# Optimization experiments

Measured on AMD Instinct MI355X. Metric: run time of the kernel, lower is better.

## Reference

```python
import jax, jax.numpy as jnp
import numpy as np

SIG_LEVEL = 2
UNIT = 128
SEQ = 64
BATCH = 256
SIG_DIM = UNIT + UNIT ** 2  # truncated signature dim for level 2
LN_EPS = 1e-5


def _signature(path, level):
    """Truncated path signature up to `level` via Chen's relation.
    path: (B, T, d) -> (B, d + d^2 + ... + d^level).
    Each segment contributes exp(dx): level-m term dx^{outer m}/m!.
    """
    B, T, d = path.shape
    dx = path[:, 1:] - path[:, :-1]  # (B, T-1, d)
    init = [jnp.zeros((B, d ** k), dtype=path.dtype) for k in range(1, level + 1)]

    def step(S, dxt):  # S: list of (B, d^k); dxt: (B, d)
        # P[m] = dxt^{outer m} / m!, flattened (B, d^m)
        P = [jnp.ones((B, 1), dtype=dxt.dtype), dxt]
        for m in range(2, level + 1):
            P.append((P[-1][:, :, None] * dxt[:, None, :]).reshape(B, d ** m) / m)
        newS = []
        for k in range(1, level + 1):
            s = P[k]  # j = 0 term (S_0 = 1)
            for j in range(1, k + 1):
                s = s + (S[j - 1][:, :, None] * P[k - j][:, None, :]).reshape(B, d ** k)
            newS.append(s)
        return newS, None

    S, _ = jax.lax.scan(step, init, jnp.swapaxes(dx, 0, 1))
    return jnp.concatenate(S, axis=-1)


def _grn_softmax(sig, W2, b2, W1, b1, Wg, bg, Wv, bv, Ws, bs, gamma, beta):
    # TFT-style gated residual network with softmax output activation.
    h = jax.nn.elu(sig @ W2 + b2)          # (B, unit)
    h = h @ W1 + b1                        # (B, unit)
    glu = jax.nn.sigmoid(h @ Wg + bg) * (h @ Wv + bv)
    skip = sig @ Ws + bs                   # residual projection sig_dim -> unit
    y = skip + glu
    mu = jnp.mean(y, axis=-1, keepdims=True)
    var = jnp.var(y, axis=-1, keepdims=True)
    y = (y - mu) * jax.lax.rsqrt(var + LN_EPS) * gamma + beta
    return jax.nn.softmax(y, axis=-1)


def setup_inputs() -> dict:
    key = jax.random.key(0)
    ks = jax.random.split(key, 16)
    s = 0.02
    return {
        "inputs": jax.random.normal(ks[0], (BATCH, SEQ, UNIT), dtype=jnp.float32),
        "time_kernel": jnp.ones((SEQ, 1), dtype=jnp.float32),
        "Wd": jax.random.normal(ks[1], (UNIT, UNIT), dtype=jnp.float32) * s,
        "bd": jnp.zeros((UNIT,), dtype=jnp.float32),
        "W2": jax.random.normal(ks[2], (SIG_DIM, UNIT), dtype=jnp.float32) * s,
        "b2": jnp.zeros((UNIT,), dtype=jnp.float32),
        "W1": jax.random.normal(ks[3], (UNIT, UNIT), dtype=jnp.float32) * s,
        "b1": jnp.zeros((UNIT,), dtype=jnp.float32),
        "Wg": jax.random.normal(ks[4], (UNIT, UNIT), dtype=jnp.float32) * s,
        "bg": jnp.zeros((UNIT,), dtype=jnp.float32),
        "Wv": jax.random.normal(ks[5], (UNIT, UNIT), dtype=jnp.float32) * s,
        "bv": jnp.zeros((UNIT,), dtype=jnp.float32),
        "Ws": jax.random.normal(ks[6], (SIG_DIM, UNIT), dtype=jnp.float32) * s,
        "bs": jnp.zeros((UNIT,), dtype=jnp.float32),
        "gamma": jnp.ones((UNIT,), dtype=jnp.float32),
        "beta": jnp.zeros((UNIT,), dtype=jnp.float32),
    }


def reference(inputs, time_kernel, Wd, bd, W2, b2, W1, b1, Wg, bg, Wv, bv, Ws, bs, gamma, beta):
    x = time_kernel * inputs                         # (B, T, d) time weighting
    sig = _signature(x, SIG_LEVEL)                   # (B, sig_dim)
    weights = _grn_softmax(sig, W2, b2, W1, b1, Wg, bg, Wv, bv, Ws, bs, gamma, beta)  # (B, d)
    dense_out = x @ Wd + bd                          # (B, T, d); dropout is identity at eval
    return dense_out * weights[:, None, :]
```

## Files before the change

kernel.cpp:

```cpp
#include <hip/hip_runtime.h>
#include <math.h>

#define SD 16512
#define NCH 32
#define NKB 516
#define RPSTRIDE 8192
#define LN_EPS 1e-5f

typedef __attribute__((ext_vector_type(4))) float f32x4;
typedef __attribute__((ext_vector_type(8))) short bf16x8;

__device__ __forceinline__ unsigned bfpack(float lo, float hi) {
    unsigned a = __builtin_bit_cast(unsigned, lo);
    unsigned b = __builtin_bit_cast(unsigned, hi);
    a = (a + 0x7FFFu + ((a >> 16) & 1u)) >> 16;
    b = (b + 0x7FFFu + ((b >> 16) & 1u)) >> 16;
    return a | (b << 16);
}
__device__ __forceinline__ unsigned short bf1(float x) {
    unsigned a = __builtin_bit_cast(unsigned, x);
    return (unsigned short)((a + 0x7FFFu + ((a >> 16) & 1u)) >> 16);
}

__global__ __launch_bounds__(512) void k_sig(const float* __restrict__ x,
                                             const float* __restrict__ tk,
                                             const float* __restrict__ Wd,
                                             const float* __restrict__ W2,
                                             const float* __restrict__ Ws,
                                             unsigned short* __restrict__ sigF,
                                             unsigned short* __restrict__ WTgF,
                                             unsigned short* __restrict__ xbf,
                                             unsigned short* __restrict__ WdTg) {
    __shared__ union {
        struct { unsigned short Ut[128][72]; unsigned short DXt[128][72]; float tks[64]; } s;
        struct { float T[32][132]; } t;
    } sm;
    int tid = threadIdx.x;
    int p = blockIdx.x;

    if (p >= 256 && p < 1288) {
        int q = p - 256;
        int mat = q & 1, kblk = q >> 1;
        int k0 = kblk * 32;
        const float* Wm = mat ? Ws : W2;
        {
            int kk = tid >> 4, c0 = (tid & 15) * 8;
            const float* src = Wm + (size_t)(k0 + kk) * 128 + c0;
            f32x4 v0 = *(const f32x4*)src;
            f32x4 v1 = *(const f32x4*)(src + 4);
            #pragma unroll
            for (int j = 0; j < 4; ++j) sm.t.T[kk][c0 + j]     = v0[j];
            #pragma unroll
            for (int j = 0; j < 4; ++j) sm.t.T[kk][c0 + 4 + j] = v1[j];
        }
        __syncthreads();
        {
            int c = tid >> 2, h8 = (tid & 3) * 8;
            uint4 o;
            o.x = bfpack(sm.t.T[h8    ][c], sm.t.T[h8 + 1][c]);
            o.y = bfpack(sm.t.T[h8 + 2][c], sm.t.T[h8 + 3][c]);
            o.z = bfpack(sm.t.T[h8 + 4][c], sm.t.T[h8 + 5][c]);
            o.w = bfpack(sm.t.T[h8 + 6][c], sm.t.T[h8 + 7][c]);
            *(uint4*)&WTgF[((size_t)(mat * NKB + kblk) * 128 + c) * 32 + h8] = o;
        }
        return;
    }
    if (p == 1288) {
        int d = tid & 127, kh = tid >> 7;
        unsigned* dst = (unsigned*)WdTg;
        for (int kk = 0; kk < 32; kk += 2) {
            int k = kh * 32 + kk;
            float v0 = Wd[(size_t)k * 128 + d];
            float v1 = Wd[(size_t)(k + 1) * 128 + d];
            dst[d * 64 + (k >> 1)] = bfpack(v0, v1);
        }
        return;
    }

    int b = p;
    if (tid < 64) sm.s.tks[tid] = tk[tid];
    __syncthreads();

    const float* xb = x + (size_t)b * 8192;
    unsigned short* xbb = xbf + (size_t)b * 8192;
    int i = tid & 127, th = tid >> 7;

    float x0 = sm.s.tks[0] * xb[i];
    float xa = sm.s.tks[th * 16] * xb[(size_t)(th * 16) * 128 + i];
    #pragma unroll
    for (int tp = 0; tp < 8; ++tp) {
        int pp = th * 8 + tp;
        int t0 = 2 * pp;
        float xv = sm.s.tks[t0 + 1] * xb[(size_t)(t0 + 1) * 128 + i];
        float dx0 = xv - xa, u0 = 0.5f * (xa + xv) - x0;
        float dx1, u1, xc;
        if (pp == 31) { dx1 = 0.f; u1 = 0.f; xc = 0.f; }
        else {
            xc = sm.s.tks[t0 + 2] * xb[(size_t)(t0 + 2) * 128 + i];
            dx1 = xc - xv; u1 = 0.5f * (xv + xc) - x0;
        }
        *(unsigned*)&sm.s.Ut[i][t0]  = bfpack(u0, u1);
        *(unsigned*)&sm.s.DXt[i][t0] = bfpack(dx0, dx1);
        xbb[(size_t)t0 * 128 + i]       = bf1(xa);
        xbb[(size_t)(t0 + 1) * 128 + i] = bf1(xv);
        if (pp == 31)
            sigF[(size_t)(i >> 5) * 8192 + b * 32 + (i & 31)] = bf1(xv - x0);
        xa = xc;
    }
    __syncthreads();

    int w = tid >> 6, lane = tid & 63;
    int wm = w >> 2, wn = w & 3;
    int l15 = lane & 15, lg = lane >> 4;
    f32x4 acc[4][2];
    #pragma unroll
    for (int m = 0; m < 4; ++m)
        #pragma unroll
        for (int n = 0; n < 2; ++n) acc[m][n] = (f32x4){0.f, 0.f, 0.f, 0.f};

    #pragma unroll
    for (int ks = 0; ks < 2; ++ks) {
        bf16x8 af[4], bfv[2];
        #pragma unroll
        for (int m = 0; m < 4; ++m)
            af[m] = *(const bf16x8*)&sm.s.Ut[wm * 64 + m * 16 + l15][ks * 32 + lg * 8];
        #pragma unroll
        for (int n = 0; n < 2; ++n)
            bfv[n] = *(const bf16x8*)&sm.s.DXt[wn * 32 + n * 16 + l15][ks * 32 + lg * 8];
        #pragma unroll
        for (int m = 0; m < 4; ++m)
            #pragma unroll
            for (int n = 0; n < 2; ++n)
                acc[m][n] = __builtin_amdgcn_mfma_f32_16x16x32_bf16(af[m], bfv[n], acc[m][n], 0, 0, 0);
    }

    #pragma unroll
    for (int m = 0; m < 4; ++m)
        #pragma unroll
        for (int n = 0; n < 2; ++n)
            #pragma unroll
            for (int rr = 0; rr < 4; ++rr) {
                int r = wm * 64 + m * 16 + lg * 4 + rr;
                sigF[(size_t)(4 * (r + 1) + wn) * 8192 + b * 32 + n * 16 + l15]
                    = bf1(acc[m][n][rr]);
            }
}

__global__ __launch_bounds__(512) void k_gemm(const unsigned short* __restrict__ sigF,
                                              const unsigned short* __restrict__ WTgF,
                                              unsigned* __restrict__ partial_p) {
    int p = blockIdx.x;
    int lid = (p & 7) * 64 + (p >> 3);
    int ch = lid >> 4;
    int mt = (lid >> 3) & 1;
    int nt = lid & 7;
    int mat = nt >> 2, ncol = (nt & 3) * 32;
    int kblk0 = ch * 16;
    int nks = (ch == 31) ? 20 : 16;

    int tid = threadIdx.x;
    int w = tid >> 6, lane = tid & 63;
    int l15 = lane & 15, lg = lane >> 4;

    const unsigned short* A = sigF + (size_t)kblk0 * 8192
                            + (size_t)(mt * 128 + w * 16 + l15) * 32 + lg * 8;
    const unsigned short* B = WTgF + ((size_t)(mat * NKB + kblk0) * 128 + ncol + l15) * 32 + lg * 8;

    f32x4 acc0 = (f32x4){0.f, 0.f, 0.f, 0.f};
    f32x4 acc1 = (f32x4){0.f, 0.f, 0.f, 0.f};

    #pragma unroll 4
    for (int ks = 0; ks < nks; ++ks) {
        bf16x8 a  = *(const bf16x8*)(A + (size_t)ks * 8192);
        bf16x8 b0 = *(const bf16x8*)(B + (size_t)ks * 4096);
        bf16x8 b1 = *(const bf16x8*)(B + (size_t)ks * 4096 + 512);
        acc0 = __builtin_amdgcn_mfma_f32_16x16x32_bf16(a, b0, acc0, 0, 0, 0);
        acc1 = __builtin_amdgcn_mfma_f32_16x16x32_bf16(a, b1, acc1, 0, 0, 0);
    }

    int r0 = mt * 128 + w * 16 + lg * 4;
    int rp0 = r0 >> 1;
    #pragma unroll
    for (int n = 0; n < 2; ++n) {
        int colg = nt * 32 + n * 16 + l15;
        f32x4 a = n ? acc1 : acc0;
        partial_p[(size_t)rp0 * RPSTRIDE + ch * 256 + colg]       = bfpack(a[0], a[1]);
        partial_p[(size_t)(rp0 + 1) * RPSTRIDE + ch * 256 + colg] = bfpack(a[2], a[3]);
    }
}

__global__ __launch_bounds__(512) void k_tail(const unsigned* __restrict__ partial_p,
                                              const unsigned short* __restrict__ xbf,
                                              const unsigned short* __restrict__ WdTg,
                                              const float* __restrict__ b2,
                                              const float* __restrict__ W1,
                                              const float* __restrict__ b1,
                                              const float* __restrict__ Wg,
                                              const float* __restrict__ bg,
                                              const float* __restrict__ Wv,
                                              const float* __restrict__ bv,
                                              const float* __restrict__ bs,
                                              const float* __restrict__ gamma,
                                              const float* __restrict__ beta,
                                              const float* __restrict__ bd,
                                              float* __restrict__ out) {
    __shared__ float hs[128], ss[128], h2s[128];
    __shared__ float red4[4][128], rtmp[2][256];
    __shared__ float wts[128];
    __shared__ float wred[2][4];

    int b = blockIdx.x, tid = threadIdx.x;
    int lane = tid & 63;
    int l15 = lane & 15, lg = lane >> 4;

    {
        int c = tid & 255, h = tid >> 8;
        float s = 0.f;
        const unsigned* Pp = partial_p + (size_t)(b >> 1) * RPSTRIDE + c;
        bool hi = (b & 1) != 0;
        #pragma unroll 8
        for (int ch = h; ch < NCH; ch += 2) {
            unsigned u = Pp[ch * 256];
            unsigned hw = hi ? (u & 0xffff0000u) : (u << 16);
            s += __builtin_bit_cast(float, hw);
        }
        rtmp[h][c] = s;
    }
    __syncthreads();
    if (tid < 256) {
        float rsum = rtmp[0][tid] + rtmp[1][tid];
        if (tid < 128) {
            float hp = rsum + b2[tid];
            hs[tid] = hp > 0.f ? hp : expm1f(hp);
        } else {
            ss[tid - 128] = rsum + bs[tid - 128];
        }
    }
    __syncthreads();

    int c = tid & 127;
    {
        int qt = tid >> 7;
        float s = 0.f;
        int kbq = qt * 32;
        #pragma unroll 8
        for (int k = 0; k < 32; ++k) s += hs[kbq + k] * W1[(size_t)(kbq + k) * 128 + c];
        red4[qt][c] = s;
    }
    __syncthreads();
    if (tid < 128)
        h2s[tid] = red4[0][tid] + red4[1][tid] + red4[2][tid] + red4[3][tid] + b1[tid];
    __syncthreads();
    {
        int idx = tid >> 7, sel = idx & 1, kh = idx >> 1;
        const float* Wx = sel ? Wv : Wg;
        float s = 0.f;
        int kbq = kh * 64;
        #pragma unroll 8
        for (int k = 0; k < 64; ++k) s += h2s[kbq + k] * Wx[(size_t)(kbq + k) * 128 + c];
        red4[idx][c] = s;
    }
    __syncthreads();

    float yv = 0.f, yn = 0.f, e = 0.f;
    if (tid < 128) {
        float g = 1.f / (1.f + expf(-(red4[0][c] + red4[2][c] + bg[c])));
        float v = red4[1][c] + red4[3][c] + bv[c];
        yv = ss[c] + g * v;
        float s1 = yv, s2 = yv * yv;
        #pragma unroll
        for (int off = 1; off < 64; off <<= 1) {
            s1 += __shfl_xor(s1, off, 64);
            s2 += __shfl_xor(s2, off, 64);
        }
        if (lane == 0) { wred[0][tid >> 6] = s1; wred[1][tid >> 6] = s2; }
    }
    __syncthreads();
    if (tid < 128) {
        float sum = wred[0][0] + wred[0][1];
        float sq  = wred[1][0] + wred[1][1];
        float mu = sum * (1.f / 128.f);
        float var = sq * (1.f / 128.f) - mu * mu;
        float rs = rsqrtf(var + LN_EPS);
        yn = (yv - mu) * rs * gamma[c] + beta[c];
        float m = yn;
        #pragma unroll
        for (int off = 1; off < 64; off <<= 1) m = fmaxf(m, __shfl_xor(m, off, 64));
        if (lane == 0) wred[0][tid >> 6] = m;
    }
    __syncthreads();
    if (tid < 128) {
        float m = fmaxf(wred[0][0], wred[0][1]);
        e = expf(yn - m);
        float s = e;
        #pragma unroll
        for (int off = 1; off < 64; off <<= 1) s += __shfl_xor(s, off, 64);
        if (lane == 0) wred[1][tid >> 6] = s;
    }
    __syncthreads();
    if (tid < 128) {
        float se = wred[1][0] + wred[1][1];
        wts[c] = e / se;
    }
    __syncthreads();

    int w4 = tid >> 6;
    const unsigned short* xrow = xbf + (size_t)b * 8192;
    f32x4 dacc[4];
    #pragma unroll
    for (int fm = 0; fm < 4; ++fm) dacc[fm] = (f32x4){0.f, 0.f, 0.f, 0.f};
    #pragma unroll
    for (int ks = 0; ks < 4; ++ks) {
        bf16x8 av[4], bv2;
        #pragma unroll
        for (int fm = 0; fm < 4; ++fm)
            av[fm] = *(const bf16x8*)(xrow + (size_t)(fm * 16 + l15) * 128 + ks * 32 + lg * 8);
        bv2 = *(const bf16x8*)(WdTg + (size_t)(w4 * 16 + l15) * 128 + ks * 32 + lg * 8);
        #pragma unroll
        for (int fm = 0; fm < 4; ++fm)
            dacc[fm] = __builtin_amdgcn_mfma_f32_16x16x32_bf16(av[fm], bv2, dacc[fm], 0, 0, 0);
    }
    int dcol = w4 * 16 + l15;
    float bdv = bd[dcol], wtv = wts[dcol];
    #pragma unroll
    for (int fm = 0; fm < 4; ++fm)
        #pragma unroll
        for (int rr = 0; rr < 4; ++rr) {
            int t = fm * 16 + lg * 4 + rr;
            out[(size_t)b * 8192 + (size_t)t * 128 + dcol] = (dacc[fm][rr] + bdv) * wtv;
        }
}

extern "C" void kernel_launch(void* const* d_in, const int* in_sizes, int n_in,
                              void* d_out, int out_size, void* d_ws, size_t ws_size,
                              hipStream_t stream) {
    const float* inputs = (const float*)d_in[0];
    const float* tk     = (const float*)d_in[1];
    const float* Wd     = (const float*)d_in[2];
    const float* bd     = (const float*)d_in[3];
    const float* W2     = (const float*)d_in[4];
    const float* b2     = (const float*)d_in[5];
    const float* W1     = (const float*)d_in[6];
    const float* b1     = (const float*)d_in[7];
    const float* Wg     = (const float*)d_in[8];
    const float* bg     = (const float*)d_in[9];
    const float* Wv     = (const float*)d_in[10];
    const float* bv     = (const float*)d_in[11];
    const float* Wsk    = (const float*)d_in[12];
    const float* bs     = (const float*)d_in[13];
    const float* gamma  = (const float*)d_in[14];
    const float* beta   = (const float*)d_in[15];
    float* out = (float*)d_out;

    char* ws = (char*)d_ws;
    unsigned short* sigF = (unsigned short*)ws;
    unsigned short* WTgF = (unsigned short*)(ws + 8454144);
    unsigned* partial_p  = (unsigned*)(ws + 16908288);
    unsigned short* xbf  = (unsigned short*)(ws + 21102592);
    unsigned short* WdTg = (unsigned short*)(ws + 25296896);

    k_sig <<<1289, 512, 0, stream>>>(inputs, tk, Wd, W2, Wsk, sigF, WTgF, xbf, WdTg);
    k_gemm<<<512, 512, 0, stream>>>(sigF, WTgF, partial_p);
    k_tail<<<256, 512, 0, stream>>>(partial_p, xbf, WdTg, b2, W1, b1, Wg, bg, Wv, bv,
                                    bs, gamma, beta, bd, out);
}
```

Baseline: 43.04 us.

## Fuse W2/Ws bf16 transpose into GEMM kernel via swizzled LDS staging

Removes the 1032 weight-conversion blocks from k_sig and the WTgF workspace. Each k_gemm block now reads its fp32 slice of W2 or Ws directly, converts it to bf16 and stores it transposed into an XOR-swizzled LDS buffer for the B operand. The intent is to drop a global write/read round trip and shrink k_sig's grid, at the cost of a serial load-and-convert prologue in each GEMM block plus higher LDS use. k_sig's batch index mapping is also permuted across blocks.

After: 40.94 us. 4.9% less time.

```diff
diff --git a/kernel.cpp b/kernel.cpp
--- a/kernel.cpp
+++ b/kernel.cpp
@@ -25,47 +25,16 @@
 __global__ __launch_bounds__(512) void k_sig(const float* __restrict__ x,
                                              const float* __restrict__ tk,
                                              const float* __restrict__ Wd,
-                                             const float* __restrict__ W2,
-                                             const float* __restrict__ Ws,
                                              unsigned short* __restrict__ sigF,
-                                             unsigned short* __restrict__ WTgF,
                                              unsigned short* __restrict__ xbf,
                                              unsigned short* __restrict__ WdTg) {
-    __shared__ union {
-        struct { unsigned short Ut[128][72]; unsigned short DXt[128][72]; float tks[64]; } s;
-        struct { float T[32][132]; } t;
-    } sm;
+    __shared__ unsigned short Ut[128][72];
+    __shared__ unsigned short DXt[128][72];
+    __shared__ float tks[64];
     int tid = threadIdx.x;
     int p = blockIdx.x;
 
-    if (p >= 256 && p < 1288) {
-        int q = p - 256;
-        int mat = q & 1, kblk = q >> 1;
-        int k0 = kblk * 32;
-        const float* Wm = mat ? Ws : W2;
-        {
-            int kk = tid >> 4, c0 = (tid & 15) * 8;
-            const float* src = Wm + (size_t)(k0 + kk) * 128 + c0;
-            f32x4 v0 = *(const f32x4*)src;
-            f32x4 v1 = *(const f32x4*)(src + 4);
-            #pragma unroll
-            for (int j = 0; j < 4; ++j) sm.t.T[kk][c0 + j]     = v0[j];
-            #pragma unroll
-            for (int j = 0; j < 4; ++j) sm.t.T[kk][c0 + 4 + j] = v1[j];
-        }
-        __syncthreads();
-        {
-            int c = tid >> 2, h8 = (tid & 3) * 8;
-            uint4 o;
-            o.x = bfpack(sm.t.T[h8    ][c], sm.t.T[h8 + 1][c]);
-            o.y = bfpack(sm.t.T[h8 + 2][c], sm.t.T[h8 + 3][c]);
-            o.z = bfpack(sm.t.T[h8 + 4][c], sm.t.T[h8 + 5][c]);
-            o.w = bfpack(sm.t.T[h8 + 6][c], sm.t.T[h8 + 7][c]);
-            *(uint4*)&WTgF[((size_t)(mat * NKB + kblk) * 128 + c) * 32 + h8] = o;
-        }
-        return;
-    }
-    if (p == 1288) {
+    if (p == 256) {
         int d = tid & 127, kh = tid >> 7;
         unsigned* dst = (unsigned*)WdTg;
         for (int kk = 0; kk < 32; kk += 2) {
@@ -77,30 +46,31 @@
         return;
     }
 
-    int b = p;
-    if (tid < 64) sm.s.tks[tid] = tk[tid];
+    int b = (p & 7) * 32 + (p >> 3);
+
+    if (tid < 64) tks[tid] = tk[tid];
     __syncthreads();
 
     const float* xb = x + (size_t)b * 8192;
     unsigned short* xbb = xbf + (size_t)b * 8192;
     int i = tid & 127, th = tid >> 7;
 
-    float x0 = sm.s.tks[0] * xb[i];
-    float xa = sm.s.tks[th * 16] * xb[(size_t)(th * 16) * 128 + i];
+    float x0 = tks[0] * xb[i];
+    float xa = tks[th * 16] * xb[(size_t)(th * 16) * 128 + i];
     #pragma unroll
     for (int tp = 0; tp < 8; ++tp) {
         int pp = th * 8 + tp;
         int t0 = 2 * pp;
-        float xv = sm.s.tks[t0 + 1] * xb[(size_t)(t0 + 1) * 128 + i];
+        float xv = tks[t0 + 1] * xb[(size_t)(t0 + 1) * 128 + i];
         float dx0 = xv - xa, u0 = 0.5f * (xa + xv) - x0;
         float dx1, u1, xc;
         if (pp == 31) { dx1 = 0.f; u1 = 0.f; xc = 0.f; }
         else {
-            xc = sm.s.tks[t0 + 2] * xb[(size_t)(t0 + 2) * 128 + i];
+            xc = tks[t0 + 2] * xb[(size_t)(t0 + 2) * 128 + i];
             dx1 = xc - xv; u1 = 0.5f * (xv + xc) - x0;
         }
-        *(unsigned*)&sm.s.Ut[i][t0]  = bfpack(u0, u1);
-        *(unsigned*)&sm.s.DXt[i][t0] = bfpack(dx0, dx1);
+        *(unsigned*)&Ut[i][t0]  = bfpack(u0, u1);
+        *(unsigned*)&DXt[i][t0] = bfpack(dx0, dx1);
         xbb[(size_t)t0 * 128 + i]       = bf1(xa);
         xbb[(size_t)(t0 + 1) * 128 + i] = bf1(xv);
         if (pp == 31)
@@ -123,10 +93,10 @@
         bf16x8 af[4], bfv[2];
         #pragma unroll
         for (int m = 0; m < 4; ++m)
-            af[m] = *(const bf16x8*)&sm.s.Ut[wm * 64 + m * 16 + l15][ks * 32 + lg * 8];
+            af[m] = *(const bf16x8*)&Ut[wm * 64 + m * 16 + l15][ks * 32 + lg * 8];
         #pragma unroll
         for (int n = 0; n < 2; ++n)
-            bfv[n] = *(const bf16x8*)&sm.s.DXt[wn * 32 + n * 16 + l15][ks * 32 + lg * 8];
+            bfv[n] = *(const bf16x8*)&DXt[wn * 32 + n * 16 + l15][ks * 32 + lg * 8];
         #pragma unroll
         for (int m = 0; m < 4; ++m)
             #pragma unroll
@@ -147,33 +117,56 @@
 }
 
 __global__ __launch_bounds__(512) void k_gemm(const unsigned short* __restrict__ sigF,
-                                              const unsigned short* __restrict__ WTgF,
+                                              const float* __restrict__ W2,
+                                              const float* __restrict__ Ws,
                                               unsigned* __restrict__ partial_p) {
+    __shared__ unsigned short Bs[32 * 640];
+
     int p = blockIdx.x;
     int lid = (p & 7) * 64 + (p >> 3);
     int ch = lid >> 4;
     int mt = (lid >> 3) & 1;
     int nt = lid & 7;
-    int mat = nt >> 2, ncol = (nt & 3) * 32;
+    const float* W = (nt < 4) ? W2 : Ws;
+    int ntc = (nt & 3) * 32;
     int kblk0 = ch * 16;
     int nks = (ch == 31) ? 20 : 16;
+    int nk = nks * 32;
+    int kb0 = kblk0 * 32;
 
     int tid = threadIdx.x;
     int w = tid >> 6, lane = tid & 63;
     int l15 = lane & 15, lg = lane >> 4;
 
+    for (int kk = tid; kk < nk; kk += 512) {
+        const float* wp = W + (size_t)(kb0 + kk) * 128 + ntc;
+        float v[32];
+        #pragma unroll
+        for (int u = 0; u < 8; ++u) {
+            f32x4 t = *(const f32x4*)(wp + u * 4);
+            v[u * 4] = t[0]; v[u * 4 + 1] = t[1]; v[u * 4 + 2] = t[2]; v[u * 4 + 3] = t[3];
+        }
+        #pragma unroll
+        for (int c = 0; c < 32; ++c) {
+            int byteoff = (c * 1280 + kk * 2) ^ ((c & 15) << 4);
+            *(unsigned short*)((char*)Bs + byteoff) = bf1(v[c]);
+        }
+    }
+    __syncthreads();
+
     const unsigned short* A = sigF + (size_t)kblk0 * 8192
                             + (size_t)(mt * 128 + w * 16 + l15) * 32 + lg * 8;
-    const unsigned short* B = WTgF + ((size_t)(mat * NKB + kblk0) * 128 + ncol + l15) * 32 + lg * 8;
 
     f32x4 acc0 = (f32x4){0.f, 0.f, 0.f, 0.f};
     f32x4 acc1 = (f32x4){0.f, 0.f, 0.f, 0.f};
 
     #pragma unroll 4
     for (int ks = 0; ks < nks; ++ks) {
-        bf16x8 a  = *(const bf16x8*)(A + (size_t)ks * 8192);
-        bf16x8 b0 = *(const bf16x8*)(B + (size_t)ks * 4096);
-        bf16x8 b1 = *(const bf16x8*)(B + (size_t)ks * 4096 + 512);
+        bf16x8 a = *(const bf16x8*)(A + (size_t)ks * 8192);
+        int kof = (ks * 32 + lg * 8) * 2;
+        int c0 = l15, c1 = 16 + l15;
+        bf16x8 b0 = *(const bf16x8*)((const char*)Bs + ((c0 * 1280 + kof) ^ ((c0 & 15) << 4)));
+        bf16x8 b1 = *(const bf16x8*)((const char*)Bs + ((c1 * 1280 + kof) ^ ((c1 & 15) << 4)));
         acc0 = __builtin_amdgcn_mfma_f32_16x16x32_bf16(a, b0, acc0, 0, 0, 0);
         acc1 = __builtin_amdgcn_mfma_f32_16x16x32_bf16(a, b1, acc1, 0, 0, 0);
     }
@@ -354,13 +347,12 @@
 
     char* ws = (char*)d_ws;
     unsigned short* sigF = (unsigned short*)ws;
-    unsigned short* WTgF = (unsigned short*)(ws + 8454144);
-    unsigned* partial_p  = (unsigned*)(ws + 16908288);
-    unsigned short* xbf  = (unsigned short*)(ws + 21102592);
-    unsigned short* WdTg = (unsigned short*)(ws + 25296896);
-
-    k_sig <<<1289, 512, 0, stream>>>(inputs, tk, Wd, W2, Wsk, sigF, WTgF, xbf, WdTg);
-    k_gemm<<<512, 512, 0, stream>>>(sigF, WTgF, partial_p);
+    unsigned* partial_p  = (unsigned*)(ws + 8454144);
+    unsigned short* xbf  = (unsigned short*)(ws + 12648448);
+    unsigned short* WdTg = (unsigned short*)(ws + 16842752);
+
+    k_sig <<<257, 512, 0, stream>>>(inputs, tk, Wd, sigF, xbf, WdTg);
+    k_gemm<<<512, 512, 0, stream>>>(sigF, W2, Wsk, partial_p);
     k_tail<<<256, 512, 0, stream>>>(partial_p, xbf, WdTg, b2, W1, b1, Wg, bg, Wv, bv,
                                     bs, gamma, beta, bd, out);
 }
```
